# Kernel tuning notes

Hardware: AMD Instinct MI355X
Metric: run time of the kernel (lower is better)

## Reference

```python
import jax, jax.numpy as jnp
import numpy as np

H, HKV, D, W = 16, 4, 128, 1024   # n_head, n_kv_head, head_dim, sliding_window_size
NE = 2048                          # n_embd
QMAX = 3.0                         # 3-bit symmetric uniform quant: codes in [-3, 3]


def _rope(x, cos, sin):
    # x: [B,T,h,D]; cos/sin: [1,T,1,D//2]
    d = x.shape[-1] // 2
    x1, x2 = x[..., :d], x[..., d:]
    return jnp.concatenate([x1 * cos + x2 * sin, -x1 * sin + x2 * cos], axis=-1)


def _rmsnorm(x):
    eps = jnp.asarray(jnp.finfo(x.dtype).eps, x.dtype)  # F.rms_norm default eps
    return x * jax.lax.rsqrt(jnp.mean(x * x, axis=-1, keepdims=True) + eps)


def _quant_dequant(x):
    # Per-(B,H,t) token symmetric uniform 3-bit scalar quantization over head_dim,
    # matching QuantizedKVCache(head_dim, bits=3): codes * scale round-trip.
    s = jnp.max(jnp.abs(x), axis=-1, keepdims=True) / QMAX
    s = jnp.maximum(s, jnp.asarray(1e-8, x.dtype))
    codes = jnp.clip(jnp.round(x / s), -QMAX, QMAX)
    return codes * s


def setup_inputs() -> dict:
    key = jax.random.key(0)
    ks = jax.random.split(key, 5)
    B, T = 1, 4096
    x = jax.random.normal(ks[0], (B, T, NE), jnp.float32)
    half = D // 2
    inv = 1.0 / (10000.0 ** (np.arange(half, dtype=np.float64) / half))
    ang = np.arange(T)[:, None] * inv[None, :]
    cos = jnp.asarray(np.cos(ang), jnp.float32)[None, :, None, :]  # [1,T,1,D/2]
    sin = jnp.asarray(np.sin(ang), jnp.float32)[None, :, None, :]
    std = 0.02
    Wq = std * jax.random.normal(ks[1], (NE, H * D), jnp.float32)
    Wk = std * jax.random.normal(ks[2], (NE, HKV * D), jnp.float32)
    Wv = std * jax.random.normal(ks[3], (NE, HKV * D), jnp.float32)
    Wo = std * jax.random.normal(ks[4], (NE, NE), jnp.float32)
    return {"x": x, "cos": cos, "sin": sin, "Wq": Wq, "Wk": Wk, "Wv": Wv, "Wo": Wo}


def reference(x, cos, sin, Wq, Wk, Wv, Wo):
    B, T, C = x.shape
    q = (x @ Wq).reshape(B, T, H, D)
    k = (x @ Wk).reshape(B, T, HKV, D)
    v = (x @ Wv).reshape(B, T, HKV, D)
    q = _rmsnorm(_rope(q, cos, sin))
    k = _rmsnorm(_rope(k, cos, sin))
    rep = H // HKV  # GQA: repeat each kv head consecutively
    k = jnp.repeat(k, rep, axis=2)
    v = jnp.repeat(v, rep, axis=2)
    q = q.transpose(0, 2, 1, 3)  # [B,H,T,D]
    k = k.transpose(0, 2, 1, 3)
    v = v.transpose(0, 2, 1, 3)
    # 3-bit quantize-dequantize KV (element-wise round trip, T > W path)
    kq = _quant_dequant(k)
    vq = _quant_dequant(v)
    nc = T // W  # number of query chunks
    KW = 2 * W - 1  # window length per chunk (kv_start = start - W + 1 .. end)
    # pad front by W-1 so every chunk's window starts at padded index chunk*W
    kp = jnp.pad(kq, ((0, 0), (0, 0), (W - 1, 0), (0, 0)))
    vp = jnp.pad(vq, ((0, 0), (0, 0), (W - 1, 0), (0, 0)))
    idx = (jnp.arange(nc) * W)[:, None] + jnp.arange(KW)[None, :]  # [nc,KW]
    kw = kp[:, :, idx]  # [B,H,nc,KW,D]
    vw = vp[:, :, idx]
    qc = q.reshape(B, H, nc, W, D)
    scale = 1.0 / np.sqrt(D)  # yarn_scale=1.0
    scores = jnp.einsum('bhcqd,bhckd->bhcqk', qc, kw) * scale  # [B,H,nc,W,KW]
    # sliding-window causal mask per chunk
    ql = jnp.arange(W)[:, None]            # local query pos
    kl = jnp.arange(KW)[None, :]           # local key pos in window
    dist = ql - kl + (W - 1)               # q_abs - k_abs
    valid = (dist >= 0) & (dist < W)       # [W,KW]
    kabs = (jnp.arange(nc) * W)[:, None] - (W - 1) + jnp.arange(KW)[None, :]  # [nc,KW]
    valid = valid[None, :, :] & (kabs[:, None, :] >= 0)  # [nc,W,KW] (drop pad)
    scores = jnp.where(valid[None, None], scores, -jnp.inf)
    attn = jax.nn.softmax(scores, axis=-1)
    out = jnp.einsum('bhcqk,bhckd->bhcqd', attn, vw)  # [B,H,nc,W,D]
    y = out.reshape(B, H, T, D).transpose(0, 2, 1, 3).reshape(B, T, C)
    return y @ Wo
```

## Files before the change

### kernel.cpp

```cpp
#include <hip/hip_runtime.h>
#include <hip/hip_bf16.h>
#include <math.h>

#define T_SEQ 4096
#define NEMB  2048
#define NH    16
#define NKV   4
#define HD    128
#define WIN   1024

typedef __attribute__((ext_vector_type(8))) __bf16 bf16x8;
typedef __attribute__((ext_vector_type(4))) __bf16 bf16x4;
typedef __attribute__((ext_vector_type(4))) float  f32x4;

#define GLOAD_LDS16(gp, lp)                                          \
  __builtin_amdgcn_global_load_lds(                                  \
      (const __attribute__((address_space(1))) void*)(gp),           \
      (__attribute__((address_space(3))) void*)(lp), 16, 0, 0)

__device__ __forceinline__ float wave_sum64(float v) {
#pragma unroll
  for (int off = 1; off < 64; off <<= 1) v += __shfl_xor(v, off, 64);
  return v;
}
__device__ __forceinline__ float wave_max64(float v) {
#pragma unroll
  for (int off = 1; off < 64; off <<= 1) v = fmaxf(v, __shfl_xor(v, off, 64));
  return v;
}
__device__ __forceinline__ uint32_t pack_bf16x2(float a, float b) {
  union { __bf16 h[2]; uint32_t u; } u_;
  u_.h[0] = (__bf16)a; u_.h[1] = (__bf16)b;
  return u_.u;
}

__global__ __launch_bounds__(256) void cast_x_split_kernel(const float* __restrict__ src,
                                                           __bf16* __restrict__ dst) {
  int i = blockIdx.x * 256 + threadIdx.x;
  int row = i >> 8, colg = i & 255;
  const f32x4* s4 = (const f32x4*)src;
  f32x4 a = s4[2 * i], b = s4[2 * i + 1];
  bf16x8 hi, lo;
#pragma unroll
  for (int j = 0; j < 4; ++j) {
    hi[j] = (__bf16)a[j]; lo[j] = (__bf16)(a[j] - (float)hi[j]);
    hi[j + 4] = (__bf16)b[j]; lo[j + 4] = (__bf16)(b[j] - (float)hi[j + 4]);
  }
  *(bf16x8*)(dst + (size_t)row * 4096 + colg * 8) = hi;
  *(bf16x8*)(dst + (size_t)row * 4096 + 2048 + colg * 8) = lo;
}

__global__ __launch_bounds__(64) void transpose_cast_kernel(const float* __restrict__ src,
                                                            __bf16* __restrict__ dst,
                                                            int K, int N) {
  int kc = blockIdx.x * 8;
  int n  = blockIdx.y * 64 + threadIdx.x;
  bf16x8 o;
#pragma unroll
  for (int j = 0; j < 8; ++j) o[j] = (__bf16)src[(size_t)(kc + j) * N + n];
  *(bf16x8*)(dst + (size_t)n * K + kc) = o;
}

__global__ __launch_bounds__(64) void transpose_split_kernel(const float* __restrict__ src,
                                                             __bf16* __restrict__ dst,
                                                             int N) {
  int kc = blockIdx.x * 8;
  int n  = blockIdx.y * 64 + threadIdx.x;
  bf16x8 hi, lo;
#pragma unroll
  for (int j = 0; j < 8; ++j) {
    float v = src[(size_t)(kc + j) * N + n];
    hi[j] = (__bf16)v; lo[j] = (__bf16)(v - (float)hi[j]);
  }
  *(bf16x8*)(dst + (size_t)n * 6144 + kc) = hi;
  *(bf16x8*)(dst + (size_t)n * 6144 + 2048 + kc) = hi;
  *(bf16x8*)(dst + (size_t)n * 6144 + 4096 + kc) = lo;
}

template <bool OUT_BF16>
__global__ __launch_bounds__(256) void gemm_kernel(const __bf16* __restrict__ A,
                                                   const __bf16* __restrict__ BT,
                                                   void* __restrict__ Cout,
                                                   int M, int N, int K,
                                                   int lda, int ldb, int awrap) {
  __shared__ __align__(16) __bf16 As[128 * 64];
  __shared__ __align__(16) __bf16 Bs[128 * 64];
  const int tid = threadIdx.x;
  const int lane = tid & 63, w = tid >> 6;
  const int wr = w >> 1, wc = w & 1;
  const int g = lane >> 4, c = lane & 15;
  const int m0 = blockIdx.y * 128, n0 = blockIdx.x * 128;
  const int srow = lane >> 3;
  const int sgrp = (lane & 7) ^ (srow & 7);
  f32x4 acc[4][4] = {};
  for (int k0 = 0; k0 < K; k0 += 64) {
    int ka = k0 + sgrp * 8;
    int kaw = (ka >= awrap) ? ka - awrap : ka;
    __syncthreads();
#pragma unroll
    for (int i = 0; i < 4; ++i) {
      int chunk = w * 4 + i;
      int row = chunk * 8 + srow;
      GLOAD_LDS16(A  + (size_t)(m0 + row) * lda + kaw, As + chunk * 512);
      GLOAD_LDS16(BT + (size_t)(n0 + row) * ldb + ka,  Bs + chunk * 512);
    }
    __syncthreads();
#pragma unroll
    for (int kk = 0; kk < 2; ++kk) {
      bf16x8 af[4], bfr[4];
#pragma unroll
      for (int mi = 0; mi < 4; ++mi) {
        int row = wr * 64 + mi * 16 + c;
        af[mi] = *(const bf16x8*)&As[row * 64 + (((kk * 4 + g) ^ (row & 7)) * 8)];
      }
#pragma unroll
      for (int ni = 0; ni < 4; ++ni) {
        int row = wc * 64 + ni * 16 + c;
        bfr[ni] = *(const bf16x8*)&Bs[row * 64 + (((kk * 4 + g) ^ (row & 7)) * 8)];
      }
#pragma unroll
      for (int mi = 0; mi < 4; ++mi)
#pragma unroll
        for (int ni = 0; ni < 4; ++ni)
          acc[mi][ni] = __builtin_amdgcn_mfma_f32_16x16x32_bf16(af[mi], bfr[ni], acc[mi][ni], 0, 0, 0);
    }
  }
#pragma unroll
  for (int mi = 0; mi < 4; ++mi) {
#pragma unroll
    for (int ni = 0; ni < 4; ++ni) {
      int row = m0 + wr * 64 + mi * 16 + g * 4;
      int col = n0 + wc * 64 + ni * 16 + c;
#pragma unroll
      for (int r = 0; r < 4; ++r) {
        if constexpr (OUT_BF16)
          ((__bf16*)Cout)[(size_t)(row + r) * N + col] = (__bf16)acc[mi][ni][r];
        else
          ((float*)Cout)[(size_t)(row + r) * N + col] = acc[mi][ni][r];
      }
    }
  }
}

__global__ __launch_bounds__(256) void rope_norm_quant_kernel(const __bf16* __restrict__ qproj,
                                                              const float* __restrict__ kvproj,
                                                              const float* __restrict__ cosp,
                                                              const float* __restrict__ sinp,
                                                              __bf16* __restrict__ qb,
                                                              __bf16* __restrict__ kb,
                                                              __bf16* __restrict__ vt) {
  const int t = blockIdx.x;
  const int w = threadIdx.x >> 6, lane = threadIdx.x & 63;
  const int slot = blockIdx.y * 4 + w;
  float a, b;
  if (slot < 16) {
    const __bf16* base = qproj + (size_t)t * 2048 + slot * 128;
    a = (float)base[lane]; b = (float)base[lane + 64];
  } else {
    const float* base = kvproj + (size_t)t * 1024 + (slot - 16) * 128;
    a = base[lane]; b = base[lane + 64];
  }
  float o1, o2;
  if (slot < 20) {
    float cv = cosp[t * 64 + lane], sv = sinp[t * 64 + lane];
    o1 = a * cv + b * sv;
    o2 = -a * sv + b * cv;
    float ss = wave_sum64(o1 * o1 + o2 * o2);
    float sc = rsqrtf(ss * (1.0f / 128.0f) + 1.1920929e-7f);
    o1 *= sc; o2 *= sc;
  } else { o1 = a; o2 = b; }
  if (slot < 16) {
    __bf16* dst = qb + ((size_t)slot * T_SEQ + t) * HD;
    dst[lane] = (__bf16)o1; dst[lane + 64] = (__bf16)o2;
  } else {
    float amax = wave_max64(fmaxf(fabsf(o1), fabsf(o2)));
    float s = fmaxf(amax * (1.0f / 3.0f), 1e-8f);
    float d1 = fminf(fmaxf(rintf(o1 / s), -3.0f), 3.0f) * s;
    float d2 = fminf(fmaxf(rintf(o2 / s), -3.0f), 3.0f) * s;
    if (slot < 20) {
      __bf16* dst = kb + ((size_t)(slot - 16) * T_SEQ + t) * HD;
      dst[lane] = (__bf16)d1; dst[lane + 64] = (__bf16)d2;
    } else {
      __bf16* dst = vt + (size_t)(slot - 20) * HD * T_SEQ;
      dst[(size_t)lane * T_SEQ + t]        = (__bf16)d1;
      dst[(size_t)(lane + 64) * T_SEQ + t] = (__bf16)d2;
    }
  }
}

__global__ __launch_bounds__(256) void attn_kernel(const __bf16* __restrict__ qb,
                                                   const __bf16* __restrict__ kb,
                                                   const __bf16* __restrict__ vt,
                                                   __bf16* __restrict__ attn) {
  const int w = threadIdx.x >> 6, lane = threadIdx.x & 63;
  const int g = lane >> 4, c = lane & 15;
  const int wg = blockIdx.x * 4 + w;
  const int h = wg >> 7, qt = wg & 127;
  const int q0 = qt * 32;
  const int hkv = h >> 2;
  const __bf16* kbase = kb + (size_t)hkv * T_SEQ * HD;
  const __bf16* vbase = vt + (size_t)hkv * HD * T_SEQ;
  const float scl = 0.08838834764831845f;

  bf16x8 qf[2][4];
#pragma unroll
  for (int mi = 0; mi < 2; ++mi)
#pragma unroll
    for (int kc = 0; kc < 4; ++kc)
      qf[mi][kc] = *(const bf16x8*)(qb + ((size_t)h * T_SEQ + q0 + 16 * mi + c) * HD + kc * 32 + 8 * g);

  f32x4 acc[2][8] = {};
  float lsum[2] = {};

  const int srcLow = ((g & 1) << 5) + c;
  const int srcHigh = srcLow + 16;
  const bool gHi = g >= 2;

  int lo = q0 - (WIN - 1);
  if (lo < 0) lo = 0;
  lo &= ~31;
  for (int kj0 = lo; kj0 <= q0 + 31; kj0 += 32) {
    bf16x8 vf[8];
#pragma unroll
    for (int df = 0; df < 8; ++df)
      vf[df] = *(const bf16x8*)(vbase + (size_t)(df * 16 + c) * T_SEQ + kj0 + 8 * g);
    f32x4 st[2][2] = {};
#pragma unroll
    for (int kc = 0; kc < 4; ++kc) {
      bf16x8 bk0 = *(const bf16x8*)(kbase + (size_t)(kj0 + c) * HD + kc * 32 + 8 * g);
      bf16x8 bk1 = *(const bf16x8*)(kbase + (size_t)(kj0 + 16 + c) * HD + kc * 32 + 8 * g);
#pragma unroll
      for (int mi = 0; mi < 2; ++mi) {
        st[0][mi] = __builtin_amdgcn_mfma_f32_16x16x32_bf16(bk0, qf[mi][kc], st[0][mi], 0, 0, 0);
        st[1][mi] = __builtin_amdgcn_mfma_f32_16x16x32_bf16(bk1, qf[mi][kc], st[1][mi], 0, 0, 0);
      }
    }
    float p[2][2][4];
#pragma unroll
    for (int ni = 0; ni < 2; ++ni)
#pragma unroll
      for (int mi = 0; mi < 2; ++mi)
#pragma unroll
        for (int r = 0; r < 4; ++r) {
          int qrow = q0 + 16 * mi + c;
          int key = kj0 + 16 * ni + 4 * g + r;
          int d = qrow - key;
          float e = __expf(st[ni][mi][r] * scl);
          p[ni][mi][r] = (d >= 0 && d < WIN) ? e : 0.0f;
        }
#pragma unroll
    for (int mi = 0; mi < 2; ++mi)
      lsum[mi] += (p[0][mi][0] + p[0][mi][1] + p[0][mi][2] + p[0][mi][3]) +
                  (p[1][mi][0] + p[1][mi][1] + p[1][mi][2] + p[1][mi][3]);
#pragma unroll
    for (int mi = 0; mi < 2; ++mi) {
      uint32_t pk00 = pack_bf16x2(p[0][mi][0], p[0][mi][1]);
      uint32_t pk01 = pack_bf16x2(p[0][mi][2], p[0][mi][3]);
      uint32_t pk10 = pack_bf16x2(p[1][mi][0], p[1][mi][1]);
      uint32_t pk11 = pack_bf16x2(p[1][mi][2], p[1][mi][3]);
      uint32_t n0a = __shfl((int)pk00, srcLow),  n0b = __shfl((int)pk01, srcLow);
      uint32_t n0c = __shfl((int)pk00, srcHigh), n0d = __shfl((int)pk01, srcHigh);
      uint32_t n1a = __shfl((int)pk10, srcLow),  n1b = __shfl((int)pk11, srcLow);
      uint32_t n1c = __shfl((int)pk10, srcHigh), n1d = __shfl((int)pk11, srcHigh);
      union { uint32_t u[4]; bf16x8 v; } bu;
      bu.u[0] = gHi ? n1a : n0a;
      bu.u[1] = gHi ? n1b : n0b;
      bu.u[2] = gHi ? n1c : n0c;
      bu.u[3] = gHi ? n1d : n0d;
#pragma unroll
      for (int df = 0; df < 8; ++df)
        acc[mi][df] = __builtin_amdgcn_mfma_f32_16x16x32_bf16(vf[df], bu.v, acc[mi][df], 0, 0, 0);
    }
  }
#pragma unroll
  for (int mi = 0; mi < 2; ++mi) {
    lsum[mi] += __shfl_xor(lsum[mi], 16, 64);
    lsum[mi] += __shfl_xor(lsum[mi], 32, 64);
    float inv = 1.0f / lsum[mi];
#pragma unroll
    for (int df = 0; df < 8; ++df) {
      bf16x4 o;
#pragma unroll
      for (int r = 0; r < 4; ++r) o[r] = (__bf16)(acc[mi][df][r] * inv);
      *(bf16x4*)(attn + (size_t)(q0 + 16 * mi + c) * NEMB + h * HD + df * 16 + 4 * g) = o;
    }
  }
}

extern "C" void kernel_launch(void* const* d_in, const int* in_sizes, int n_in,
                              void* d_out, int out_size, void* d_ws, size_t ws_size,
                              hipStream_t stream) {
  (void)in_sizes; (void)n_in; (void)out_size; (void)ws_size;
  const float* x    = (const float*)d_in[0];
  const float* cosp = (const float*)d_in[1];
  const float* sinp = (const float*)d_in[2];
  const float* Wq   = (const float*)d_in[3];
  const float* Wk   = (const float*)d_in[4];
  const float* Wv   = (const float*)d_in[5];
  const float* Wo   = (const float*)d_in[6];

  char* ws = (char*)d_ws;
  __bf16* xsplit = (__bf16*)(ws + 0);
  __bf16* qproj  = (__bf16*)(ws + 33554432);
  float*  kvproj = (float*)(ws + 50331648);
  __bf16* wqT    = (__bf16*)(ws + 67108864);
  __bf16* wkvT   = (__bf16*)(ws + 75497472);
  __bf16* wot    = (__bf16*)(ws + 88080384);
  __bf16* qbuf   = (__bf16*)(ws + 96468992);
  __bf16* kbuf   = (__bf16*)(ws + 113246208);
  __bf16* vbuf   = (__bf16*)(ws + 117440512);
  __bf16* abuf   = (__bf16*)(ws + 0);

  cast_x_split_kernel<<<4096, 256, 0, stream>>>(x, xsplit);
  transpose_cast_kernel<<<dim3(256, 32), 64, 0, stream>>>(Wq, wqT, 2048, 2048);
  transpose_split_kernel<<<dim3(256, 8), 64, 0, stream>>>(Wk, wkvT, 512);
  transpose_split_kernel<<<dim3(256, 8), 64, 0, stream>>>(Wv, wkvT + (size_t)512 * 6144, 512);
  transpose_cast_kernel<<<dim3(256, 32), 64, 0, stream>>>(Wo, wot, 2048, 2048);

  gemm_kernel<true><<<dim3(16, 32), 256, 0, stream>>>(xsplit, wqT, qproj,
                                                      4096, 2048, 2048, 4096, 2048, 1 << 30);
  gemm_kernel<false><<<dim3(8, 32), 256, 0, stream>>>(xsplit, wkvT, kvproj,
                                                      4096, 1024, 6144, 4096, 6144, 4096);
  rope_norm_quant_kernel<<<dim3(4096, 6), 256, 0, stream>>>(qproj, kvproj, cosp, sinp,
                                                            qbuf, kbuf, vbuf);
  attn_kernel<<<512, 256, 0, stream>>>(qbuf, kbuf, vbuf, abuf);
  gemm_kernel<false><<<dim3(16, 32), 256, 0, stream>>>(abuf, wot, d_out,
                                                       4096, 2048, 2048, 2048, 2048, 1 << 30);
}
```

Measured before the change: 514.4 us.

## Share K/V tiles across waves via double-buffered LDS, narrow GEMM tiles, swizzle blocks

```diff
diff --git a/kernel.cpp b/kernel.cpp
--- a/kernel.cpp
+++ b/kernel.cpp
@@ -77,19 +77,24 @@
   *(bf16x8*)(dst + (size_t)n * 6144 + 4096 + kc) = lo;
 }
 
-template <bool OUT_BF16>
+template <bool OUT_BF16, int BN>
 __global__ __launch_bounds__(256) void gemm_kernel(const __bf16* __restrict__ A,
                                                    const __bf16* __restrict__ BT,
                                                    void* __restrict__ Cout,
                                                    int M, int N, int K,
                                                    int lda, int ldb, int awrap) {
+  constexpr int NI = BN / 32;
   __shared__ __align__(16) __bf16 As[128 * 64];
-  __shared__ __align__(16) __bf16 Bs[128 * 64];
+  __shared__ __align__(16) __bf16 Bs[BN * 64];
   const int tid = threadIdx.x;
   const int lane = tid & 63, w = tid >> 6;
   const int wr = w >> 1, wc = w & 1;
   const int g = lane >> 4, c = lane & 15;
-  const int m0 = blockIdx.y * 128, n0 = blockIdx.x * 128;
+  const int nwg = gridDim.x * gridDim.y;
+  int idx = blockIdx.y * gridDim.x + blockIdx.x;
+  idx = (idx & 7) * (nwg >> 3) + (idx >> 3);
+  const int bx = idx % gridDim.x, by = idx / gridDim.x;
+  const int m0 = by * 128, n0 = bx * BN;
   const int srow = lane >> 3;
   const int sgrp = (lane & 7) ^ (srow & 7);
   f32x4 acc[4][4] = {};
@@ -101,36 +106,41 @@
     for (int i = 0; i < 4; ++i) {
       int chunk = w * 4 + i;
       int row = chunk * 8 + srow;
-      GLOAD_LDS16(A  + (size_t)(m0 + row) * lda + kaw, As + chunk * 512);
-      GLOAD_LDS16(BT + (size_t)(n0 + row) * ldb + ka,  Bs + chunk * 512);
+      GLOAD_LDS16(A + (size_t)(m0 + row) * lda + kaw, As + chunk * 512);
+    }
+#pragma unroll
+    for (int i = 0; i < NI; ++i) {
+      int chunk = w * NI + i;
+      int row = chunk * 8 + srow;
+      GLOAD_LDS16(BT + (size_t)(n0 + row) * ldb + ka, Bs + chunk * 512);
     }
     __syncthreads();
 #pragma unroll
     for (int kk = 0; kk < 2; ++kk) {
-      bf16x8 af[4], bfr[4];
+      bf16x8 af[4], bfr[NI];
 #pragma unroll
       for (int mi = 0; mi < 4; ++mi) {
         int row = wr * 64 + mi * 16 + c;
         af[mi] = *(const bf16x8*)&As[row * 64 + (((kk * 4 + g) ^ (row & 7)) * 8)];
       }
 #pragma unroll
-      for (int ni = 0; ni < 4; ++ni) {
-        int row = wc * 64 + ni * 16 + c;
+      for (int ni = 0; ni < NI; ++ni) {
+        int row = wc * (BN / 2) + ni * 16 + c;
         bfr[ni] = *(const bf16x8*)&Bs[row * 64 + (((kk * 4 + g) ^ (row & 7)) * 8)];
       }
 #pragma unroll
       for (int mi = 0; mi < 4; ++mi)
 #pragma unroll
-        for (int ni = 0; ni < 4; ++ni)
+        for (int ni = 0; ni < NI; ++ni)
           acc[mi][ni] = __builtin_amdgcn_mfma_f32_16x16x32_bf16(af[mi], bfr[ni], acc[mi][ni], 0, 0, 0);
     }
   }
 #pragma unroll
   for (int mi = 0; mi < 4; ++mi) {
 #pragma unroll
-    for (int ni = 0; ni < 4; ++ni) {
+    for (int ni = 0; ni < NI; ++ni) {
       int row = m0 + wr * 64 + mi * 16 + g * 4;
-      int col = n0 + wc * 64 + ni * 16 + c;
+      int col = n0 + wc * (BN / 2) + ni * 16 + c;
 #pragma unroll
       for (int r = 0; r < 4; ++r) {
         if constexpr (OUT_BF16)
@@ -192,11 +202,14 @@
                                                    const __bf16* __restrict__ kb,
                                                    const __bf16* __restrict__ vt,
                                                    __bf16* __restrict__ attn) {
+  __shared__ __align__(16) __bf16 Ks[2][32 * 128];
+  __shared__ __align__(16) __bf16 Vs[2][128 * 32];
   const int w = threadIdx.x >> 6, lane = threadIdx.x & 63;
   const int g = lane >> 4, c = lane & 15;
-  const int wg = blockIdx.x * 4 + w;
-  const int h = wg >> 7, qt = wg & 127;
-  const int q0 = qt * 32;
+  const int bid = (blockIdx.x & 7) * 64 + (blockIdx.x >> 3);
+  const int h = bid >> 5, st = bid & 31;
+  const int Q0 = st * 128;
+  const int q0 = Q0 + 32 * w;
   const int hkv = h >> 2;
   const __bf16* kbase = kb + (size_t)hkv * T_SEQ * HD;
   const __bf16* vbase = vt + (size_t)hkv * HD * T_SEQ;
@@ -216,61 +229,90 @@
   const int srcHigh = srcLow + 16;
   const bool gHi = g >= 2;
 
-  int lo = q0 - (WIN - 1);
+  int lo = Q0 - (WIN - 1);
   if (lo < 0) lo = 0;
   lo &= ~31;
-  for (int kj0 = lo; kj0 <= q0 + 31; kj0 += 32) {
-    bf16x8 vf[8];
-#pragma unroll
-    for (int df = 0; df < 8; ++df)
-      vf[df] = *(const bf16x8*)(vbase + (size_t)(df * 16 + c) * T_SEQ + kj0 + 8 * g);
-    f32x4 st[2][2] = {};
-#pragma unroll
-    for (int kc = 0; kc < 4; ++kc) {
-      bf16x8 bk0 = *(const bf16x8*)(kbase + (size_t)(kj0 + c) * HD + kc * 32 + 8 * g);
-      bf16x8 bk1 = *(const bf16x8*)(kbase + (size_t)(kj0 + 16 + c) * HD + kc * 32 + 8 * g);
+  const int kjEnd = Q0 + 96;
+
+  auto stage = [&](int buf, int kj0) {
+#pragma unroll
+    for (int cl = 0; cl < 2; ++cl) {
+      int s0 = cl * 256 + w * 64;
+      int s = s0 + lane;
+      int krow = s >> 4, kgl = s & 15;
+      GLOAD_LDS16(kbase + (size_t)(kj0 + krow) * HD + ((kgl ^ (krow & 7)) << 3),
+                  &Ks[buf][(size_t)s0 * 8]);
+      int vd = s >> 2, vgl = s & 3;
+      GLOAD_LDS16(vbase + (size_t)vd * T_SEQ + kj0 + ((vgl ^ (vd & 3)) << 3),
+                  &Vs[buf][(size_t)s0 * 8]);
+    }
+  };
+
+  stage(0, lo);
+  asm volatile("s_waitcnt vmcnt(0)" ::: "memory");
+  __syncthreads();
+  int cur = 0;
+  for (int kj0 = lo; kj0 <= kjEnd; kj0 += 32) {
+    if (kj0 < kjEnd) stage(cur ^ 1, kj0 + 32);
+    if (kj0 >= q0 - 1054 && kj0 <= q0 + 31) {
+      bf16x8 vf[8];
+#pragma unroll
+      for (int df = 0; df < 8; ++df) {
+        int d = df * 16 + c;
+        vf[df] = *(const bf16x8*)&Vs[cur][d * 32 + ((g ^ (d & 3)) << 3)];
+      }
+      f32x4 st_[2][2] = {};
+#pragma unroll
+      for (int kc = 0; kc < 4; ++kc) {
+        int r0 = c, r1 = 16 + c;
+        bf16x8 bk0 = *(const bf16x8*)&Ks[cur][r0 * 128 + (((4 * kc + g) ^ (r0 & 7)) << 3)];
+        bf16x8 bk1 = *(const bf16x8*)&Ks[cur][r1 * 128 + (((4 * kc + g) ^ (r1 & 7)) << 3)];
+#pragma unroll
+        for (int mi = 0; mi < 2; ++mi) {
+          st_[0][mi] = __builtin_amdgcn_mfma_f32_16x16x32_bf16(bk0, qf[mi][kc], st_[0][mi], 0, 0, 0);
+          st_[1][mi] = __builtin_amdgcn_mfma_f32_16x16x32_bf16(bk1, qf[mi][kc], st_[1][mi], 0, 0, 0);
+        }
+      }
+      float p[2][2][4];
+#pragma unroll
+      for (int ni = 0; ni < 2; ++ni)
+#pragma unroll
+        for (int mi = 0; mi < 2; ++mi)
+#pragma unroll
+          for (int r = 0; r < 4; ++r) {
+            int qrow = q0 + 16 * mi + c;
+            int key = kj0 + 16 * ni + 4 * g + r;
+            int d = qrow - key;
+            float e = __expf(st_[ni][mi][r] * scl);
+            p[ni][mi][r] = (d >= 0 && d < WIN) ? e : 0.0f;
+          }
+#pragma unroll
+      for (int mi = 0; mi < 2; ++mi)
+        lsum[mi] += (p[0][mi][0] + p[0][mi][1] + p[0][mi][2] + p[0][mi][3]) +
+                    (p[1][mi][0] + p[1][mi][1] + p[1][mi][2] + p[1][mi][3]);
 #pragma unroll
       for (int mi = 0; mi < 2; ++mi) {
-        st[0][mi] = __builtin_amdgcn_mfma_f32_16x16x32_bf16(bk0, qf[mi][kc], st[0][mi], 0, 0, 0);
-        st[1][mi] = __builtin_amdgcn_mfma_f32_16x16x32_bf16(bk1, qf[mi][kc], st[1][mi], 0, 0, 0);
-      }
-    }
-    float p[2][2][4];
-#pragma unroll
-    for (int ni = 0; ni < 2; ++ni)
-#pragma unroll
-      for (int mi = 0; mi < 2; ++mi)
-#pragma unroll
-        for (int r = 0; r < 4; ++r) {
-          int qrow = q0 + 16 * mi + c;
-          int key = kj0 + 16 * ni + 4 * g + r;
-          int d = qrow - key;
-          float e = __expf(st[ni][mi][r] * scl);
-          p[ni][mi][r] = (d >= 0 && d < WIN) ? e : 0.0f;
-        }
-#pragma unroll
-    for (int mi = 0; mi < 2; ++mi)
-      lsum[mi] += (p[0][mi][0] + p[0][mi][1] + p[0][mi][2] + p[0][mi][3]) +
-                  (p[1][mi][0] + p[1][mi][1] + p[1][mi][2] + p[1][mi][3]);
-#pragma unroll
-    for (int mi = 0; mi < 2; ++mi) {
-      uint32_t pk00 = pack_bf16x2(p[0][mi][0], p[0][mi][1]);
-      uint32_t pk01 = pack_bf16x2(p[0][mi][2], p[0][mi][3]);
-      uint32_t pk10 = pack_bf16x2(p[1][mi][0], p[1][mi][1]);
-      uint32_t pk11 = pack_bf16x2(p[1][mi][2], p[1][mi][3]);
-      uint32_t n0a = __shfl((int)pk00, srcLow),  n0b = __shfl((int)pk01, srcLow);
-      uint32_t n0c = __shfl((int)pk00, srcHigh), n0d = __shfl((int)pk01, srcHigh);
-      uint32_t n1a = __shfl((int)pk10, srcLow),  n1b = __shfl((int)pk11, srcLow);
-      uint32_t n1c = __shfl((int)pk10, srcHigh), n1d = __shfl((int)pk11, srcHigh);
-      union { uint32_t u[4]; bf16x8 v; } bu;
-      bu.u[0] = gHi ? n1a : n0a;
-      bu.u[1] = gHi ? n1b : n0b;
-      bu.u[2] = gHi ? n1c : n0c;
-      bu.u[3] = gHi ? n1d : n0d;
-#pragma unroll
-      for (int df = 0; df < 8; ++df)
-        acc[mi][df] = __builtin_amdgcn_mfma_f32_16x16x32_bf16(vf[df], bu.v, acc[mi][df], 0, 0, 0);
-    }
+        uint32_t pk00 = pack_bf16x2(p[0][mi][0], p[0][mi][1]);
+        uint32_t pk01 = pack_bf16x2(p[0][mi][2], p[0][mi][3]);
+        uint32_t pk10 = pack_bf16x2(p[1][mi][0], p[1][mi][1]);
+        uint32_t pk11 = pack_bf16x2(p[1][mi][2], p[1][mi][3]);
+        uint32_t n0a = __shfl((int)pk00, srcLow),  n0b = __shfl((int)pk01, srcLow);
+        uint32_t n0c = __shfl((int)pk00, srcHigh), n0d = __shfl((int)pk01, srcHigh);
+        uint32_t n1a = __shfl((int)pk10, srcLow),  n1b = __shfl((int)pk11, srcLow);
+        uint32_t n1c = __shfl((int)pk10, srcHigh), n1d = __shfl((int)pk11, srcHigh);
+        union { uint32_t u[4]; bf16x8 v; } bu;
+        bu.u[0] = gHi ? n1a : n0a;
+        bu.u[1] = gHi ? n1b : n0b;
+        bu.u[2] = gHi ? n1c : n0c;
+        bu.u[3] = gHi ? n1d : n0d;
+#pragma unroll
+        for (int df = 0; df < 8; ++df)
+          acc[mi][df] = __builtin_amdgcn_mfma_f32_16x16x32_bf16(vf[df], bu.v, acc[mi][df], 0, 0, 0);
+      }
+    }
+    asm volatile("s_waitcnt vmcnt(0)" ::: "memory");
+    __syncthreads();
+    cur ^= 1;
   }
 #pragma unroll
   for (int mi = 0; mi < 2; ++mi) {
@@ -317,13 +359,13 @@
   transpose_split_kernel<<<dim3(256, 8), 64, 0, stream>>>(Wv, wkvT + (size_t)512 * 6144, 512);
   transpose_cast_kernel<<<dim3(256, 32), 64, 0, stream>>>(Wo, wot, 2048, 2048);
 
-  gemm_kernel<true><<<dim3(16, 32), 256, 0, stream>>>(xsplit, wqT, qproj,
-                                                      4096, 2048, 2048, 4096, 2048, 1 << 30);
-  gemm_kernel<false><<<dim3(8, 32), 256, 0, stream>>>(xsplit, wkvT, kvproj,
-                                                      4096, 1024, 6144, 4096, 6144, 4096);
+  gemm_kernel<true, 64><<<dim3(32, 32), 256, 0, stream>>>(xsplit, wqT, qproj,
+                                                          4096, 2048, 2048, 4096, 2048, 1 << 30);
+  gemm_kernel<false, 64><<<dim3(16, 32), 256, 0, stream>>>(xsplit, wkvT, kvproj,
+                                                           4096, 1024, 6144, 4096, 6144, 4096);
   rope_norm_quant_kernel<<<dim3(4096, 6), 256, 0, stream>>>(qproj, kvproj, cosp, sinp,
                                                             qbuf, kbuf, vbuf);
   attn_kernel<<<512, 256, 0, stream>>>(qbuf, kbuf, vbuf, abuf);
-  gemm_kernel<false><<<dim3(16, 32), 256, 0, stream>>>(abuf, wot, d_out,
-                                                       4096, 2048, 2048, 2048, 2048, 1 << 30);
-}
+  gemm_kernel<false, 64><<<dim3(32, 32), 256, 0, stream>>>(abuf, wot, d_out,
+                                                           4096, 2048, 2048, 2048, 2048, 1 << 30);
+}
```

Result: faster. 434.7 us (-15.5%).
